# Kernel optimization log

Hardware: AMD Instinct MI355X
Metric: run time of the kernel (lower is better)

The kernel has to match this reference:

```python
import jax, jax.numpy as jnp
import numpy as np
from jax import lax

B, N, T, E, HE, HD, NE = 512, 100, 100, 128, 64, 256, 512
BETA = 0.25


def setup_inputs() -> dict:
    key = jax.random.key(0)
    ks = jax.random.split(key, 16)
    f32 = jnp.float32
    x = jax.random.normal(ks[0], (B, N, T), f32)
    traj_mask = (jax.random.uniform(ks[1], (B, N, T)) > 0.1).astype(f32)
    instance_mask = (jax.random.uniform(ks[2], (B, N)) > 0.2).astype(f32)

    def w_init(k, shape, fan_in):
        return (jax.random.normal(k, shape, f32) / np.sqrt(fan_in)).astype(f32)

    params = dict(
        conv1_w=w_init(ks[3], (HE, 2, 3), 2 * 3), conv1_b=jnp.zeros((HE,), f32),
        conv2_w=w_init(ks[4], (HE, HE, 3), HE * 3), conv2_b=jnp.zeros((HE,), f32),
        lat_w=w_init(ks[5], (E, HE), HE), lat_b=jnp.zeros((E,), f32),
        codebook=(jax.random.uniform(ks[6], (NE, E), f32) * 2.0 - 1.0) / NE,
        d1_w=w_init(ks[7], (HD, E), E), d1_b=jnp.zeros((HD,), f32),
        d2_w=w_init(ks[8], (HD, HD), HD), d2_b=jnp.zeros((HD,), f32),
        d3_w=w_init(ks[9], (T, HD), HD), d3_b=jnp.zeros((T,), f32),
    )
    return {"x": x, "traj_mask": traj_mask, "instance_mask": instance_mask, **params}


def _conv1d(h, w, b):
    # h: (M, C_in, L), w: (C_out, C_in, K) -> (M, C_out, L), padding=1 == SAME for K=3
    y = lax.conv_general_dilated(h, w, (1,), 'SAME', dimension_numbers=('NCH', 'OIH', 'NCH'))
    return jax.nn.relu(y + b[None, :, None])


def reference(x, traj_mask, instance_mask, conv1_w, conv1_b, conv2_w, conv2_b,
              lat_w, lat_b, codebook, d1_w, d1_b, d2_w, d2_b, d3_w, d3_b):
    b, n, t = x.shape
    steps = t // 2
    im = instance_mask[..., None]  # (B,N,1)

    # ---- encode (masked input) ----
    x_in = x * traj_mask * im
    h = x_in.reshape(b * n, steps, 2).transpose(0, 2, 1)  # (M, 2, steps)
    h = _conv1d(h, conv1_w, conv1_b)
    h = _conv1d(h, conv2_w, conv2_b)
    h = h.mean(axis=-1)                                   # (M, HE)
    z = (h @ lat_w.T + lat_b).reshape(b, n, -1)           # (B, N, E)
    z = z * im

    # ---- vector quantize (nbooks=1), quant_prop=1.0 ----
    zf = z.reshape(-1, z.shape[-1])                       # (M, E)
    d = ((zf * zf).sum(-1, keepdims=True)
         - 2.0 * zf @ codebook.T
         + (codebook * codebook).sum(-1))                 # (M, NE)
    idx = jnp.argmin(d, axis=-1)                          # (M,)
    zq = codebook[idx]                                    # (M, E) gather
    sg = lax.stop_gradient
    vq_loss = (BETA * jnp.mean((zf - sg(zq)) ** 2, -1)
               + jnp.mean((sg(zf) - zq) ** 2, -1)).reshape(b, n)
    zq = zf + sg(zq - zf)                                 # straight-through
    z_q = zq.reshape(b, n, -1)

    # ---- apply instance mask to VQ outputs ----
    denom = jnp.maximum(instance_mask.sum(), 1.0)
    vq_reduced = (vq_loss * instance_mask).sum() / denom
    indices = idx.reshape(b, n, 1)
    indices = jnp.where(im > 0, indices, jnp.full_like(indices, -1))
    z_q = z_q * im

    # ---- decode ----
    h2 = jax.nn.relu(z_q.reshape(b * n, -1) @ d1_w.T + d1_b)
    h2 = jax.nn.relu(h2 @ d2_w.T + d2_b)
    x_hat = (h2 @ d3_w.T + d3_b).reshape(b, n, t)

    # ---- masked reconstruction loss ----
    recon_w = im * traj_mask
    recon_loss = (((x_hat - x) ** 2) * recon_w).sum() / jnp.maximum(recon_w.sum(), 1.0)
    return x_hat, recon_loss, vq_reduced, indices
```

## Files before the change

### kernel.cpp

```cpp
#include <hip/hip_runtime.h>
#include <stdint.h>

typedef unsigned long long u64;
typedef unsigned short ushort_t;
typedef __attribute__((ext_vector_type(8))) short short8;
typedef __attribute__((ext_vector_type(8))) _Float16 half8;
typedef __attribute__((ext_vector_type(16))) float f32x16;


#define WS_RNP0     0ll
#define WS_RNP1     51200ll
#define WS_ZHI      102400ll
#define WS_ZLO      3379200ll
#define WS_ENCBHI   6656000ll
#define WS_ENCBLO   6662144ll
#define WS_CBHI     6668288ll
#define WS_CBLO     6701056ll
#define WS_CBNORM   6733824ll
#define WS_D1F      6734336ll
#define WS_D2F      6750720ll
#define WS_D3F      6783488ll
#define WS_ACCUMS   6799872ll
#define WS_GBEST    6799880ll
#define WS_H1       6902280ll
#define WS_H2       13455880ll

__device__ __host__ inline ushort_t bf16_rn(float v) {
  unsigned u = __float_as_uint(v);
  unsigned r = (u + 0x7fffu + ((u >> 16) & 1u)) >> 16;
  return (ushort_t)r;
}
union h2u { _Float16 h; unsigned short u; };
union s2h { short8 s; half8 h; };

__device__ inline unsigned pk2_bf16(float a, float b) {
  unsigned r;
  asm("v_cvt_pk_bf16_f32 %0, %1, %2" : "=v"(r) : "v"(a), "v"(b));
  return r;
}

__device__ inline int rowfn(int r, int half) { return (r & 3) + 8*(r >> 2) + 4*half; }

#define MFMA_BF16 __builtin_amdgcn_mfma_f32_32x32x16_bf16

__global__ __launch_bounds__(256) void prep_kernel(
    const float* __restrict__ w2, const float* __restrict__ cb,
    const float* __restrict__ d1w, const float* __restrict__ d2w,
    const float* __restrict__ d3w,
    ushort_t* __restrict__ ebhi, ushort_t* __restrict__ eblo,
    ushort_t* __restrict__ cbhi, ushort_t* __restrict__ cblo,
    ushort_t* __restrict__ d1f, ushort_t* __restrict__ d2f,
    ushort_t* __restrict__ d3f, float* __restrict__ cbnorm)
{
  const int total = 12288 + 65536 + 32768 + 65536 + 32768 + 512;
  for (int i = blockIdx.x*256 + threadIdx.x; i < total; i += gridDim.x*256) {
    int idx = i;
    if (idx < 12288) {
      int j = idx & 7, l6 = (idx >> 3) & 63, f = idx >> 9;
      int kt = f & 3, ntt = (f >> 2) & 1, t = f >> 3;
      int oc = ntt*32 + (l6 & 31);
      int ic = kt*16 + (l6 >> 5)*8 + j;
      float v = w2[(oc*64 + ic)*3 + t];
      ushort_t hi = bf16_rn(v);
      float hf = __uint_as_float(((unsigned)hi) << 16);
      ebhi[idx] = hi; eblo[idx] = bf16_rn(v - hf); continue;
    }
    idx -= 12288;
    if (idx < 65536) {
      int j = idx & 7, l6 = (idx >> 3) & 63, f = idx >> 9;
      int kt = f & 7, ntg = f >> 3;
      int k = kt*16 + (l6 >> 5)*8 + j;
      int n = ntg*32 + (l6 & 31);
      float v = cb[n*128 + k] * 512.0f;
      h2u a, b; a.h = (_Float16)v;
      b.h = (_Float16)(v - (float)a.h);
      cbhi[idx] = a.u; cblo[idx] = b.u; continue;
    }
    idx -= 65536;
    if (idx < 32768) {
      int j = idx & 7, l6 = (idx >> 3) & 63, f = idx >> 9;
      int kt = f & 7, ntg = f >> 3;
      int k = kt*16 + (l6 >> 5)*8 + j;
      int n = ntg*32 + (l6 & 31);
      d1f[idx] = bf16_rn(d1w[n*128 + k]); continue;
    }
    idx -= 32768;
    if (idx < 65536) {
      int j = idx & 7, l6 = (idx >> 3) & 63, f = idx >> 9;
      int kt = f & 15, ntg = f >> 4;
      int k = kt*16 + (l6 >> 5)*8 + j;
      int n = ntg*32 + (l6 & 31);
      d2f[idx] = bf16_rn(d2w[n*256 + k]); continue;
    }
    idx -= 65536;
    if (idx < 32768) {
      int j = idx & 7, l6 = (idx >> 3) & 63, f = idx >> 9;
      int kt = f & 15, ntg = f >> 4;
      int k = kt*16 + (l6 >> 5)*8 + j;
      int n = ntg*32 + (l6 & 31);
      d3f[idx] = (n < 100) ? bf16_rn(d3w[n*256 + k]) : (ushort_t)0; continue;
    }
    idx -= 32768;
    { double s = 0.0; const float* c = cb + idx*128;
      for (int e = 0; e < 128; ++e) { double v = (double)c[e]; s += v*v; }
      cbnorm[idx] = (float)s; }
  }
}

__global__ __launch_bounds__(256, 3) void encoder_kernel(
    const float* __restrict__ x, const float* __restrict__ tm,
    const float* __restrict__ imask,
    const float* w1, const float* b1,
    const ushort_t* __restrict__ ebhi, const ushort_t* __restrict__ eblo,
    const float* b2, float* __restrict__ red)
{
  __shared__ ushort_t s_H[4][52*128];
  const int tid  = threadIdx.x;
  const int wv   = __builtin_amdgcn_readfirstlane((int)(tid >> 6));
  const int lane = tid & 63;
  const int ln31 = lane & 31, half = lane >> 5;
  const long m   = (long)blockIdx.x*4 + wv;
  const float imv = imask[m];
  ushort_t* Hw  = s_H[wv];

  {
    const int p = (lane < 50) ? lane : 0;
    const long xb = m*100 + 2*p;
    const float2 x0v = *(const float2*)(x + xb);
    const float2 t0v = *(const float2*)(tm + xb);
    float2 xmv = {0.f, 0.f}, tmv = {0.f, 0.f};
    float2 xpv = {0.f, 0.f}, tpv = {0.f, 0.f};
    if (p > 0)  { xmv = *(const float2*)(x + xb - 2); tmv = *(const float2*)(tm + xb - 2); }
    if (p < 49) { xpv = *(const float2*)(x + xb + 2); tpv = *(const float2*)(tm + xb + 2); }
    const float a0 = xmv.x*tmv.x, c0 = xmv.y*tmv.y;
    const float a1 = x0v.x*t0v.x, c1 = x0v.y*t0v.y;
    const float a2 = xpv.x*tpv.x, c2 = xpv.y*tpv.y;
    const int row = lane + 1;
    const int sw  = (row & 7) << 4;
    char* rbase = (char*)(Hw + row*128);
    #pragma unroll
    for (int g = 0; g < 4; ++g) {
      unsigned hi8[8], lo8[8];
      #pragma unroll
      for (int pr = 0; pr < 8; ++pr) {
        const int o = g*16 + pr*2;
        const float* wA = w1 + (long)o*6;
        const float* wB = wA + 6;
        float sA = 0.f, sB = 0.f;
        sA = fmaf(wA[0], a0, sA); sA = fmaf(wA[1], a1, sA); sA = fmaf(wA[2], a2, sA);
        sA = fmaf(wA[3], c0, sA); sA = fmaf(wA[4], c1, sA); sA = fmaf(wA[5], c2, sA);
        sB = fmaf(wB[0], a0, sB); sB = fmaf(wB[1], a1, sB); sB = fmaf(wB[2], a2, sB);
        sB = fmaf(wB[3], c0, sB); sB = fmaf(wB[4], c1, sB); sB = fmaf(wB[5], c2, sB);
        const float hA = fmaxf(fmaf(imv, sA, b1[o]),     0.f);
        const float hB = fmaxf(fmaf(imv, sB, b1[o + 1]), 0.f);
        const unsigned h = pk2_bf16(hA, hB);
        const float ha = __uint_as_float(h << 16);
        const float hb = __uint_as_float(h & 0xffff0000u);
        lo8[pr] = pk2_bf16(hA - ha, hB - hb);
        hi8[pr] = h;
      }
      if (lane < 50) {
        *(short8*)(rbase + ((g*32)       ^ sw)) = *(short8*)&hi8[0];
        *(short8*)(rbase + ((g*32 + 16)  ^ sw)) = *(short8*)&hi8[4];
        *(short8*)(rbase + (128 + ((g*32)      ^ sw))) = *(short8*)&lo8[0];
        *(short8*)(rbase + (128 + ((g*32 + 16) ^ sw))) = *(short8*)&lo8[4];
      }
    }
    if (lane == 50 || lane == 51) {
      const int zr = (lane == 50) ? 0 : 51;
      short8 z8 = {};
      short8* d = (short8*)(Hw + zr*128);
      #pragma unroll
      for (int i = 0; i < 16; ++i) d[i] = z8;
    }
  }
  asm volatile("s_waitcnt lgkmcnt(0)" ::: "memory");
  __builtin_amdgcn_sched_barrier(0);

  f32x16 acc00, acc01, acc10, acc11;
  #pragma unroll
  for (int q = 0; q < 16; ++q) { acc00[q] = 0.f; acc01[q] = 0.f; acc10[q] = 0.f; acc11[q] = 0.f; }
  {
    const short8* bh8 = (const short8*)ebhi;
    const short8* bl8 = (const short8*)eblo;
    for (int t = 0; t < 3; ++t) {
      const int r0 = ln31 + t;
      int r1 = 32 + ln31 + t;
      if (r1 > 51) r1 = 51;
      const int sw0 = (r0 & 7) << 4, sw1 = (r1 & 7) << 4;
      const char* b0p = (const char*)(Hw + r0*128);
      const char* b1p = (const char*)(Hw + r1*128);
      #pragma unroll
      for (int kt = 0; kt < 4; ++kt) {
        const int f0 = (t*2 + 0)*4 + kt;
        const int f1 = (t*2 + 1)*4 + kt;
        const int offh = kt*32 + half*16;
        const short8 Bh0 = bh8[f0*64 + lane], Bl0 = bl8[f0*64 + lane];
        const short8 Bh1 = bh8[f1*64 + lane], Bl1 = bl8[f1*64 + lane];
        const short8 ah0 = *(const short8*)(b0p + (offh ^ sw0));
        const short8 al0 = *(const short8*)(b0p + (128 + (offh ^ sw0)));
        const short8 ah1 = *(const short8*)(b1p + (offh ^ sw1));
        const short8 al1 = *(const short8*)(b1p + (128 + (offh ^ sw1)));
        acc00 = MFMA_BF16(ah0, Bh0, acc00, 0, 0, 0);
        acc00 = MFMA_BF16(ah0, Bl0, acc00, 0, 0, 0);
        acc00 = MFMA_BF16(al0, Bh0, acc00, 0, 0, 0);
        acc01 = MFMA_BF16(ah0, Bh1, acc01, 0, 0, 0);
        acc01 = MFMA_BF16(ah0, Bl1, acc01, 0, 0, 0);
        acc01 = MFMA_BF16(al0, Bh1, acc01, 0, 0, 0);
        acc10 = MFMA_BF16(ah1, Bh0, acc10, 0, 0, 0);
        acc10 = MFMA_BF16(ah1, Bl0, acc10, 0, 0, 0);
        acc10 = MFMA_BF16(al1, Bh0, acc10, 0, 0, 0);
        acc11 = MFMA_BF16(ah1, Bh1, acc11, 0, 0, 0);
        acc11 = MFMA_BF16(ah1, Bl1, acc11, 0, 0, 0);
        acc11 = MFMA_BF16(al1, Bh1, acc11, 0, 0, 0);
      }
    }
  }

  {
    const float bv0 = b2[ln31];
    const float bv1 = b2[32 + ln31];
    float s0 = 0.f, s1 = 0.f;
    #pragma unroll
    for (int r = 0; r < 16; ++r) {
      s0 += fmaxf(acc00[r] + bv0, 0.f);
      s1 += fmaxf(acc01[r] + bv1, 0.f);
      const int mpos = 32 + rowfn(r, half);
      const float v10 = fmaxf(acc10[r] + bv0, 0.f);
      const float v11 = fmaxf(acc11[r] + bv1, 0.f);
      if (mpos < 50) { s0 += v10; s1 += v11; }
    }
    s0 += __shfl_xor(s0, 32);
    s1 += __shfl_xor(s1, 32);
    if (half == 0) {
      red[m*64 + ln31]      = s0;
      red[m*64 + 32 + ln31] = s1;
    }
  }
}

__global__ __launch_bounds__(256, 4) void latent_kernel(
    const float* __restrict__ red, const float* __restrict__ imask,
    const float* __restrict__ latw, const float* __restrict__ latb,
    ushort_t* __restrict__ zhi, ushort_t* __restrict__ zlo,
    float* __restrict__ rnp0, float* __restrict__ rnp1)
{
  __shared__ float s_r[64*64];
  __shared__ float s_im[64];
  const int tid = threadIdx.x;
  const long m0 = (long)blockIdx.x * 64;
  {
    const int r = tid >> 2, seg = tid & 3;
    const float4* src = (const float4*)(red + (m0 + r)*64 + seg*16);
    float4* dst = (float4*)(s_r + r*64 + seg*16);
    dst[0] = src[0]; dst[1] = src[1]; dst[2] = src[2]; dst[3] = src[3];
  }
  if (tid < 64) s_im[tid] = imask[m0 + tid];
  __syncthreads();

  const int e = tid & 127, mh = tid >> 7;
  const int lane = tid & 63;
  float4 W[16];
  const float4* wp = (const float4*)(latw + (long)e*64);
  #pragma unroll
  for (int q = 0; q < 16; ++q) W[q] = wp[q];
  const float lb = latb[e];

  for (int i = 0; i < 32; ++i) {
    const int ml = mh*32 + i;
    const float4* rp = (const float4*)(s_r + ml*64);
    float a = 0.f;
    #pragma unroll
    for (int q = 0; q < 16; ++q) {
      const float4 r4 = rp[q];
      a = fmaf(W[q].x, r4.x, a); a = fmaf(W[q].y, r4.y, a);
      a = fmaf(W[q].z, r4.z, a); a = fmaf(W[q].w, r4.w, a);
    }
    const float z = fmaf(0.02f, a, lb) * s_im[ml];
    h2u zh, zl; zh.h = (_Float16)z; zl.h = (_Float16)(z - (float)zh.h);
    const long mg = m0 + ml;
    zhi[mg*128 + e] = zh.u;
    zlo[mg*128 + e] = zl.u;
    float v = z*z;
    #pragma unroll
    for (int off = 32; off > 0; off >>= 1) v += __shfl_down(v, off);
    if (lane == 0) { if (e < 64) rnp0[mg] = v; else rnp1[mg] = v; }
  }
}

__global__ __launch_bounds__(256) void vq_kernel(
    const ushort_t* __restrict__ zhi, const ushort_t* __restrict__ zlo,
    const ushort_t* __restrict__ cbhi, const ushort_t* __restrict__ cblo,
    const float* __restrict__ rnp0, const float* __restrict__ rnp1,
    const float* __restrict__ cbnorm, u64* __restrict__ gbest)
{
  __shared__ ushort_t s_ah[32*136];
  __shared__ ushort_t s_al[32*136];
  __shared__ float s_rn[32];
  __shared__ u64 s_best[32];
  const int tid = threadIdx.x;
  const int m0 = blockIdx.x * 32;
  {
    const short8* gh = (const short8*)(zhi + (long)m0*128);
    const short8* gl = (const short8*)(zlo + (long)m0*128);
    const int row = tid >> 3, c8 = (tid & 7)*2;
    ((short8*)s_ah)[row*17 + c8]     = gh[tid*2];
    ((short8*)s_ah)[row*17 + c8 + 1] = gh[tid*2 + 1];
    ((short8*)s_al)[row*17 + c8]     = gl[tid*2];
    ((short8*)s_al)[row*17 + c8 + 1] = gl[tid*2 + 1];
  }
  if (tid < 32) { s_rn[tid] = rnp0[m0 + tid] + rnp1[m0 + tid]; s_best[tid] = ~0ULL; }
  __syncthreads();

  const int wv = tid >> 6, lane = tid & 63;
  const int ln31 = lane & 31, half = lane >> 5;
  float rnv[16];
  #pragma unroll
  for (int r = 0; r < 16; ++r) rnv[r] = s_rn[rowfn(r, half)];

  u64 best[16];
  #pragma unroll
  for (int r = 0; r < 16; ++r) best[r] = ~0ULL;

  const short8* ch8 = (const short8*)cbhi;
  const short8* cl8 = (const short8*)cblo;
  for (int ct = 0; ct < 4; ++ct) {
    const int ntg = wv*4 + ct;
    half8 Bh[8], Bl[8];
    #pragma unroll
    for (int kt = 0; kt < 8; ++kt) {
      s2h a, b;
      a.s = ch8[(ntg*8 + kt)*64 + lane];
      b.s = cl8[(ntg*8 + kt)*64 + lane];
      Bh[kt] = a.h; Bl[kt] = b.h;
    }
    f32x16 acc;
    #pragma unroll
    for (int q = 0; q < 16; ++q) acc[q] = 0.f;
    const int base8 = ln31*17 + half;
    #pragma unroll
    for (int kt = 0; kt < 8; ++kt) {
      s2h ah, al;
      ah.s = ((const short8*)s_ah)[base8 + kt*2];
      al.s = ((const short8*)s_al)[base8 + kt*2];
      acc = __builtin_amdgcn_mfma_f32_32x32x16_f16(ah.h, Bh[kt], acc, 0, 0, 0);
      acc = __builtin_amdgcn_mfma_f32_32x32x16_f16(ah.h, Bl[kt], acc, 0, 0, 0);
      acc = __builtin_amdgcn_mfma_f32_32x32x16_f16(al.h, Bh[kt], acc, 0, 0, 0);
    }
    const int code = ntg*32 + ln31;
    const float nrm = cbnorm[code];
    #pragma unroll
    for (int r = 0; r < 16; ++r) {
      const float t = fmaf(-0.00390625f, acc[r], rnv[r]);
      const float d = t + nrm;
      const u64 pk = ((u64)__float_as_uint(d) << 32) | (u64)(unsigned)code;
      if (pk < best[r]) best[r] = pk;
    }
  }
  #pragma unroll
  for (int r = 0; r < 16; ++r) atomicMin(&s_best[rowfn(r, half)], best[r]);
  __syncthreads();
  if (tid < 32) gbest[m0 + tid] = s_best[tid];
}

__global__ __launch_bounds__(256) void dec1_kernel(
    const float* __restrict__ cb, const u64* __restrict__ gbest,
    const float* __restrict__ imask, const ushort_t* __restrict__ bfrag,
    const float* __restrict__ bias, ushort_t* __restrict__ h1out,
    float* __restrict__ out_idx, float* __restrict__ accums)
{
  __shared__ ushort_t s_a[64*136];
  __shared__ int s_idx[64];
  __shared__ float s_act[64];
  const int tid = threadIdx.x;
  const long m0 = (long)blockIdx.x * 64;
  if (tid < 64) {
    const u64 pk = gbest[m0 + tid];
    const int ii = (int)(unsigned)(pk & 0xffffffffULL);
    const float dd = __uint_as_float((unsigned)(pk >> 32));
    const float imv = imask[m0 + tid];
    s_idx[tid] = ii; s_act[tid] = imv;
    out_idx[m0 + tid] = (imv > 0.f) ? (float)ii : -1.0f;
    float vqp = 1.25f * dd * (1.0f/128.0f) * imv;
    float sim = imv;
    #pragma unroll
    for (int off = 32; off > 0; off >>= 1) {
      vqp += __shfl_down(vqp, off); sim += __shfl_down(sim, off);
    }
    if (tid == 0) { atomicAdd(&accums[1], vqp); atomicAdd(&accums[3], sim); }
  }
  __syncthreads();
  {
    const int row = tid >> 2, seg = tid & 3;
    const float4* src = (const float4*)(cb + (long)s_idx[row]*128 + seg*32);
    const float im = s_act[row];
    ushort_t tmp[32];
    #pragma unroll
    for (int q = 0; q < 8; ++q) {
      const float4 v = src[q];
      tmp[q*4+0] = bf16_rn(v.x*im); tmp[q*4+1] = bf16_rn(v.y*im);
      tmp[q*4+2] = bf16_rn(v.z*im); tmp[q*4+3] = bf16_rn(v.w*im);
    }
    short8* dst = (short8*)(s_a + row*136 + seg*32);
    #pragma unroll
    for (int q = 0; q < 4; ++q) dst[q] = *(short8*)&tmp[q*8];
  }
  __syncthreads();
  const int wv = tid >> 6, lane = tid & 63;
  const int ln31 = lane & 31, half = lane >> 5;
  const short8* bf = (const short8*)bfrag;
  #pragma unroll
  for (int nti = 0; nti < 2; ++nti) {
    const int ntg = wv + nti*4;
    short8 B[8];
    #pragma unroll
    for (int kt = 0; kt < 8; ++kt) B[kt] = bf[(ntg*8 + kt)*64 + lane];
    const float bv = bias[ntg*32 + ln31];
    #pragma unroll
    for (int mtl = 0; mtl < 2; ++mtl) {
      f32x16 acc;
      #pragma unroll
      for (int q = 0; q < 16; ++q) acc[q] = 0.f;
      const int base8 = (mtl*32 + ln31)*17 + half;
      #pragma unroll
      for (int kt = 0; kt < 8; ++kt) {
        const short8 a = ((const short8*)s_a)[base8 + kt*2];
        acc = MFMA_BF16(a, B[kt], acc, 0, 0, 0);
      }
      const int col = ntg*32 + ln31;
      #pragma unroll
      for (int r = 0; r < 16; ++r) {
        const long row = m0 + mtl*32 + rowfn(r, half);
        h1out[row*256 + col] = bf16_rn(fmaxf(acc[r] + bv, 0.f));
      }
    }
  }
}

__global__ __launch_bounds__(256) void dec2_kernel(
    const ushort_t* __restrict__ ain, const ushort_t* __restrict__ bfrag,
    const float* __restrict__ bias, ushort_t* __restrict__ outbuf)
{
  __shared__ ushort_t s_a[64*264];
  const int tid = threadIdx.x;
  const long m0 = (long)blockIdx.x * 64;
  {
    const int row = tid >> 2, seg = tid & 3;
    const short8* src = (const short8*)(ain + (m0 + row)*256 + seg*64);
    short8* dst = (short8*)(s_a + row*264 + seg*64);
    #pragma unroll
    for (int q = 0; q < 8; ++q) dst[q] = src[q];
  }
  __syncthreads();
  const int wv = tid >> 6, lane = tid & 63;
  const int ln31 = lane & 31, half = lane >> 5;
  const short8* bf = (const short8*)bfrag;
  #pragma unroll
  for (int nti = 0; nti < 2; ++nti) {
    const int ntg = wv + nti*4;
    short8 B[16];
    #pragma unroll
    for (int kt = 0; kt < 16; ++kt) B[kt] = bf[(ntg*16 + kt)*64 + lane];
    const float bv = bias[ntg*32 + ln31];
    #pragma unroll
    for (int mtl = 0; mtl < 2; ++mtl) {
      f32x16 acc;
      #pragma unroll
      for (int q = 0; q < 16; ++q) acc[q] = 0.f;
      const int base8 = (mtl*32 + ln31)*33 + half;
      #pragma unroll
      for (int kt = 0; kt < 16; ++kt) {
        const short8 a = ((const short8*)s_a)[base8 + kt*2];
        acc = MFMA_BF16(a, B[kt], acc, 0, 0, 0);
      }
      const int col = ntg*32 + ln31;
      #pragma unroll
      for (int r = 0; r < 16; ++r) {
        const long row = m0 + mtl*32 + rowfn(r, half);
        outbuf[row*256 + col] = bf16_rn(fmaxf(acc[r] + bv, 0.f));
      }
    }
  }
}

__global__ __launch_bounds__(256) void dec3_kernel(
    const ushort_t* __restrict__ ain, const ushort_t* __restrict__ bfrag,
    const float* __restrict__ bias, const float* __restrict__ x,
    const float* __restrict__ tm, const float* __restrict__ imask,
    float* __restrict__ xhat, float* __restrict__ accums)
{
  __shared__ ushort_t s_a[64*264];
  const int tid = threadIdx.x;
  const long m0 = (long)blockIdx.x * 64;
  {
    const int row = tid >> 2, seg = tid & 3;
    const short8* src = (const short8*)(ain + (m0 + row)*256 + seg*64);
    short8* dst = (short8*)(s_a + row*264 + seg*64);
    #pragma unroll
    for (int q = 0; q < 8; ++q) dst[q] = src[q];
  }
  __syncthreads();
  const int wv = tid >> 6, lane = tid & 63;
  const int ln31 = lane & 31, half = lane >> 5;
  const short8* bf = (const short8*)bfrag;
  const int ntg = wv;
  short8 B[16];
  #pragma unroll
  for (int kt = 0; kt < 16; ++kt) B[kt] = bf[(ntg*16 + kt)*64 + lane];
  const int col = ntg*32 + ln31;
  const float bv = (col < 100) ? bias[col] : 0.f;
  float part = 0.f, wsum = 0.f;
  #pragma unroll
  for (int mtl = 0; mtl < 2; ++mtl) {
    f32x16 acc;
    #pragma unroll
    for (int q = 0; q < 16; ++q) acc[q] = 0.f;
    const int base8 = (mtl*32 + ln31)*33 + half;
    #pragma unroll
    for (int kt = 0; kt < 16; ++kt) {
      const short8 a = ((const short8*)s_a)[base8 + kt*2];
      acc = MFMA_BF16(a, B[kt], acc, 0, 0, 0);
    }
    if (col < 100) {
      #pragma unroll
      for (int r = 0; r < 16; ++r) {
        const long row = m0 + mtl*32 + rowfn(r, half);
        const float xh = acc[r] + bv;
        xhat[row*100 + col] = xh;
        const float wgt = imask[row] * tm[row*100 + col];
        const float df = xh - x[row*100 + col];
        part = fmaf(df*df, wgt, part);
        wsum += wgt;
      }
    }
  }
  #pragma unroll
  for (int off = 32; off > 0; off >>= 1) {
    part += __shfl_down(part, off); wsum += __shfl_down(wsum, off);
  }
  __shared__ float s_p[4], s_w[4];
  if (lane == 0) { s_p[wv] = part; s_w[wv] = wsum; }
  __syncthreads();
  if (tid == 0) {
    atomicAdd(&accums[0], s_p[0]+s_p[1]+s_p[2]+s_p[3]);
    atomicAdd(&accums[2], s_w[0]+s_w[1]+s_w[2]+s_w[3]);
  }
}

__global__ void finalize_kernel(const float* __restrict__ accums, float* __restrict__ out) {
  if (threadIdx.x == 0 && blockIdx.x == 0) {
    out[5120000] = accums[0] / fmaxf(accums[2], 1.0f);
    out[5120001] = accums[1] / fmaxf(accums[3], 1.0f);
  }
}

extern "C" void kernel_launch(void* const* d_in, const int* in_sizes, int n_in,
                              void* d_out, int out_size, void* d_ws, size_t ws_size,
                              hipStream_t stream)
{
  (void)in_sizes; (void)n_in; (void)out_size; (void)ws_size;
  const float* x     = (const float*)d_in[0];
  const float* tmsk  = (const float*)d_in[1];
  const float* imask = (const float*)d_in[2];
  const float* w1    = (const float*)d_in[3];
  const float* b1    = (const float*)d_in[4];
  const float* w2    = (const float*)d_in[5];
  const float* b2    = (const float*)d_in[6];
  const float* latw  = (const float*)d_in[7];
  const float* latb  = (const float*)d_in[8];
  const float* cb    = (const float*)d_in[9];
  const float* d1w   = (const float*)d_in[10];
  const float* d1b   = (const float*)d_in[11];
  const float* d2w   = (const float*)d_in[12];
  const float* d2b   = (const float*)d_in[13];
  const float* d3w   = (const float*)d_in[14];
  const float* d3b   = (const float*)d_in[15];
  float* out = (float*)d_out;
  float* ws  = (float*)d_ws;

  float*    rnp0   = ws + WS_RNP0;
  float*    rnp1   = ws + WS_RNP1;
  ushort_t* zhi    = (ushort_t*)(ws + WS_ZHI);
  ushort_t* zlo    = (ushort_t*)(ws + WS_ZLO);
  ushort_t* ebhi   = (ushort_t*)(ws + WS_ENCBHI);
  ushort_t* eblo   = (ushort_t*)(ws + WS_ENCBLO);
  ushort_t* cbhi   = (ushort_t*)(ws + WS_CBHI);
  ushort_t* cblo   = (ushort_t*)(ws + WS_CBLO);
  float*    cbnorm = ws + WS_CBNORM;
  ushort_t* d1f    = (ushort_t*)(ws + WS_D1F);
  ushort_t* d2f    = (ushort_t*)(ws + WS_D2F);
  ushort_t* d3f    = (ushort_t*)(ws + WS_D3F);
  float*    accums = ws + WS_ACCUMS;
  u64*      gbest  = (u64*)(ws + WS_GBEST);
  ushort_t* h1     = (ushort_t*)(ws + WS_H1);
  ushort_t* h2     = (ushort_t*)(ws + WS_H2);
  float*    red    = ws + WS_H1;
  float* xhat    = out;
  float* out_idx = out + 5120002;

  hipMemsetAsync(accums, 0, 8*sizeof(float), stream);

  prep_kernel<<<512, 256, 0, stream>>>(w2, cb, d1w, d2w, d3w,
                                       ebhi, eblo, cbhi, cblo, d1f, d2f, d3f, cbnorm);
  encoder_kernel<<<12800, 256, 0, stream>>>(x, tmsk, imask, w1, b1, ebhi, eblo, b2, red);
  latent_kernel<<<800, 256, 0, stream>>>(red, imask, latw, latb, zhi, zlo, rnp0, rnp1);
  vq_kernel<<<1600, 256, 0, stream>>>(zhi, zlo, cbhi, cblo, rnp0, rnp1, cbnorm, gbest);
  dec1_kernel<<<800, 256, 0, stream>>>(cb, gbest, imask, d1f, d1b, h1, out_idx, accums);
  dec2_kernel<<<800, 256, 0, stream>>>(h1, d2f, d2b, h2);
  dec3_kernel<<<800, 256, 0, stream>>>(h2, d3f, d3b, x, tmsk, imask, xhat, accums);
  finalize_kernel<<<1, 64, 0, stream>>>(accums, out);
}
```

Measured before the change: 479.8 us.

## Fuse three decoder GEMM kernels into one LDS-resident decoder kernel

Merges dec1, dec2 and dec3 into a single kernel that keeps the 64-row h1 and h2 activations in shared memory instead of writing and rereading them through global memory, which also removes two kernel launches. It also changes the encoder's LDS swizzle to XOR bit 7 by row, so the lo-half stores and loads sit in a different bank pattern and may conflict less. The fused kernel uses about 67KB of LDS per block and declares a minimum of two blocks per CU, which may limit occupancy compared with the separate kernels.

```diff
diff --git a/kernel.cpp b/kernel.cpp
--- a/kernel.cpp
+++ b/kernel.cpp
@@ -22,8 +22,7 @@
 #define WS_D3F      6783488ll
 #define WS_ACCUMS   6799872ll
 #define WS_GBEST    6799880ll
-#define WS_H1       6902280ll
-#define WS_H2       13455880ll
+#define WS_RED      6902280ll
 
 __device__ __host__ inline ushort_t bf16_rn(float v) {
   unsigned u = __float_as_uint(v);
@@ -136,7 +135,7 @@
     const float a1 = x0v.x*t0v.x, c1 = x0v.y*t0v.y;
     const float a2 = xpv.x*tpv.x, c2 = xpv.y*tpv.y;
     const int row = lane + 1;
-    const int sw  = (row & 7) << 4;
+    const int sw  = ((row & 7) << 4) | (((row >> 3) & 1) << 7);
     char* rbase = (char*)(Hw + row*128);
     #pragma unroll
     for (int g = 0; g < 4; ++g) {
@@ -160,10 +159,10 @@
         hi8[pr] = h;
       }
       if (lane < 50) {
-        *(short8*)(rbase + ((g*32)       ^ sw)) = *(short8*)&hi8[0];
-        *(short8*)(rbase + ((g*32 + 16)  ^ sw)) = *(short8*)&hi8[4];
-        *(short8*)(rbase + (128 + ((g*32)      ^ sw))) = *(short8*)&lo8[0];
-        *(short8*)(rbase + (128 + ((g*32 + 16) ^ sw))) = *(short8*)&lo8[4];
+        *(short8*)(rbase + ((g*32)        ^ sw)) = *(short8*)&hi8[0];
+        *(short8*)(rbase + ((g*32 + 16)   ^ sw)) = *(short8*)&hi8[4];
+        *(short8*)(rbase + ((g*32 + 128)  ^ sw)) = *(short8*)&lo8[0];
+        *(short8*)(rbase + ((g*32 + 144)  ^ sw)) = *(short8*)&lo8[4];
       }
     }
     if (lane == 50 || lane == 51) {
@@ -187,7 +186,8 @@
       const int r0 = ln31 + t;
       int r1 = 32 + ln31 + t;
       if (r1 > 51) r1 = 51;
-      const int sw0 = (r0 & 7) << 4, sw1 = (r1 & 7) << 4;
+      const int sw0 = ((r0 & 7) << 4) | (((r0 >> 3) & 1) << 7);
+      const int sw1 = ((r1 & 7) << 4) | (((r1 >> 3) & 1) << 7);
       const char* b0p = (const char*)(Hw + r0*128);
       const char* b1p = (const char*)(Hw + r1*128);
       #pragma unroll
@@ -198,9 +198,9 @@
         const short8 Bh0 = bh8[f0*64 + lane], Bl0 = bl8[f0*64 + lane];
         const short8 Bh1 = bh8[f1*64 + lane], Bl1 = bl8[f1*64 + lane];
         const short8 ah0 = *(const short8*)(b0p + (offh ^ sw0));
-        const short8 al0 = *(const short8*)(b0p + (128 + (offh ^ sw0)));
+        const short8 al0 = *(const short8*)(b0p + ((offh + 128) ^ sw0));
         const short8 ah1 = *(const short8*)(b1p + (offh ^ sw1));
-        const short8 al1 = *(const short8*)(b1p + (128 + (offh ^ sw1)));
+        const short8 al1 = *(const short8*)(b1p + ((offh + 128) ^ sw1));
         acc00 = MFMA_BF16(ah0, Bh0, acc00, 0, 0, 0);
         acc00 = MFMA_BF16(ah0, Bl0, acc00, 0, 0, 0);
         acc00 = MFMA_BF16(al0, Bh0, acc00, 0, 0, 0);
@@ -363,17 +363,24 @@
   if (tid < 32) gbest[m0 + tid] = s_best[tid];
 }
 
-__global__ __launch_bounds__(256) void dec1_kernel(
+__global__ __launch_bounds__(256, 2) void decoder_kernel(
     const float* __restrict__ cb, const u64* __restrict__ gbest,
-    const float* __restrict__ imask, const ushort_t* __restrict__ bfrag,
-    const float* __restrict__ bias, ushort_t* __restrict__ h1out,
-    float* __restrict__ out_idx, float* __restrict__ accums)
+    const float* __restrict__ imask,
+    const ushort_t* __restrict__ d1frag, const float* __restrict__ d1b,
+    const ushort_t* __restrict__ d2frag, const float* __restrict__ d2b,
+    const ushort_t* __restrict__ d3frag, const float* __restrict__ d3b,
+    const float* __restrict__ x, const float* __restrict__ tm,
+    float* __restrict__ xhat, float* __restrict__ out_idx,
+    float* __restrict__ accums)
 {
-  __shared__ ushort_t s_a[64*136];
+  __shared__ ushort_t s_u[64*264];
+  __shared__ ushort_t s_h1[64*264];
   __shared__ int s_idx[64];
   __shared__ float s_act[64];
+  __shared__ float s_p[4], s_w[4];
   const int tid = threadIdx.x;
   const long m0 = (long)blockIdx.x * 64;
+
   if (tid < 64) {
     const u64 pk = gbest[m0 + tid];
     const int ii = (int)(unsigned)(pk & 0xffffffffULL);
@@ -401,149 +408,120 @@
       tmp[q*4+0] = bf16_rn(v.x*im); tmp[q*4+1] = bf16_rn(v.y*im);
       tmp[q*4+2] = bf16_rn(v.z*im); tmp[q*4+3] = bf16_rn(v.w*im);
     }
-    short8* dst = (short8*)(s_a + row*136 + seg*32);
+    short8* dst = (short8*)(s_u + row*136 + seg*32);
     #pragma unroll
     for (int q = 0; q < 4; ++q) dst[q] = *(short8*)&tmp[q*8];
   }
   __syncthreads();
+
   const int wv = tid >> 6, lane = tid & 63;
   const int ln31 = lane & 31, half = lane >> 5;
-  const short8* bf = (const short8*)bfrag;
-  #pragma unroll
-  for (int nti = 0; nti < 2; ++nti) {
-    const int ntg = wv + nti*4;
-    short8 B[8];
-    #pragma unroll
-    for (int kt = 0; kt < 8; ++kt) B[kt] = bf[(ntg*8 + kt)*64 + lane];
-    const float bv = bias[ntg*32 + ln31];
+
+  {
+    const short8* bf = (const short8*)d1frag;
+    #pragma unroll
+    for (int nti = 0; nti < 2; ++nti) {
+      const int ntg = wv + nti*4;
+      short8 B[8];
+      #pragma unroll
+      for (int kt = 0; kt < 8; ++kt) B[kt] = bf[(ntg*8 + kt)*64 + lane];
+      const float bv = d1b[ntg*32 + ln31];
+      #pragma unroll
+      for (int mtl = 0; mtl < 2; ++mtl) {
+        f32x16 acc;
+        #pragma unroll
+        for (int q = 0; q < 16; ++q) acc[q] = 0.f;
+        const int base8 = (mtl*32 + ln31)*17 + half;
+        #pragma unroll
+        for (int kt = 0; kt < 8; ++kt) {
+          const short8 a = ((const short8*)s_u)[base8 + kt*2];
+          acc = MFMA_BF16(a, B[kt], acc, 0, 0, 0);
+        }
+        const int col = ntg*32 + ln31;
+        #pragma unroll
+        for (int r = 0; r < 16; ++r) {
+          const int row = mtl*32 + rowfn(r, half);
+          s_h1[row*264 + col] = bf16_rn(fmaxf(acc[r] + bv, 0.f));
+        }
+      }
+    }
+  }
+  __syncthreads();
+
+  {
+    const short8* bf = (const short8*)d2frag;
+    #pragma unroll
+    for (int nti = 0; nti < 2; ++nti) {
+      const int ntg = wv + nti*4;
+      short8 B[16];
+      #pragma unroll
+      for (int kt = 0; kt < 16; ++kt) B[kt] = bf[(ntg*16 + kt)*64 + lane];
+      const float bv = d2b[ntg*32 + ln31];
+      #pragma unroll
+      for (int mtl = 0; mtl < 2; ++mtl) {
+        f32x16 acc;
+        #pragma unroll
+        for (int q = 0; q < 16; ++q) acc[q] = 0.f;
+        const int base8 = (mtl*32 + ln31)*33 + half;
+        #pragma unroll
+        for (int kt = 0; kt < 16; ++kt) {
+          const short8 a = ((const short8*)s_h1)[base8 + kt*2];
+          acc = MFMA_BF16(a, B[kt], acc, 0, 0, 0);
+        }
+        const int col = ntg*32 + ln31;
+        #pragma unroll
+        for (int r = 0; r < 16; ++r) {
+          const int row = mtl*32 + rowfn(r, half);
+          s_u[row*264 + col] = bf16_rn(fmaxf(acc[r] + bv, 0.f));
+        }
+      }
+    }
+  }
+  __syncthreads();
+
+  {
+    const short8* bf = (const short8*)d3frag;
+    const int ntg = wv;
+    short8 B[16];
+    #pragma unroll
+    for (int kt = 0; kt < 16; ++kt) B[kt] = bf[(ntg*16 + kt)*64 + lane];
+    const int col = ntg*32 + ln31;
+    const float bv = (col < 100) ? d3b[col] : 0.f;
+    float part = 0.f, wsum = 0.f;
     #pragma unroll
     for (int mtl = 0; mtl < 2; ++mtl) {
       f32x16 acc;
       #pragma unroll
       for (int q = 0; q < 16; ++q) acc[q] = 0.f;
-      const int base8 = (mtl*32 + ln31)*17 + half;
-      #pragma unroll
-      for (int kt = 0; kt < 8; ++kt) {
-        const short8 a = ((const short8*)s_a)[base8 + kt*2];
+      const int base8 = (mtl*32 + ln31)*33 + half;
+      #pragma unroll
+      for (int kt = 0; kt < 16; ++kt) {
+        const short8 a = ((const short8*)s_u)[base8 + kt*2];
         acc = MFMA_BF16(a, B[kt], acc, 0, 0, 0);
       }
-      const int col = ntg*32 + ln31;
-      #pragma unroll
-      for (int r = 0; r < 16; ++r) {
-        const long row = m0 + mtl*32 + rowfn(r, half);
-        h1out[row*256 + col] = bf16_rn(fmaxf(acc[r] + bv, 0.f));
-      }
-    }
-  }
-}
-
-__global__ __launch_bounds__(256) void dec2_kernel(
-    const ushort_t* __restrict__ ain, const ushort_t* __restrict__ bfrag,
-    const float* __restrict__ bias, ushort_t* __restrict__ outbuf)
-{
-  __shared__ ushort_t s_a[64*264];
-  const int tid = threadIdx.x;
-  const long m0 = (long)blockIdx.x * 64;
-  {
-    const int row = tid >> 2, seg = tid & 3;
-    const short8* src = (const short8*)(ain + (m0 + row)*256 + seg*64);
-    short8* dst = (short8*)(s_a + row*264 + seg*64);
-    #pragma unroll
-    for (int q = 0; q < 8; ++q) dst[q] = src[q];
-  }
-  __syncthreads();
-  const int wv = tid >> 6, lane = tid & 63;
-  const int ln31 = lane & 31, half = lane >> 5;
-  const short8* bf = (const short8*)bfrag;
-  #pragma unroll
-  for (int nti = 0; nti < 2; ++nti) {
-    const int ntg = wv + nti*4;
-    short8 B[16];
-    #pragma unroll
-    for (int kt = 0; kt < 16; ++kt) B[kt] = bf[(ntg*16 + kt)*64 + lane];
-    const float bv = bias[ntg*32 + ln31];
-    #pragma unroll
-    for (int mtl = 0; mtl < 2; ++mtl) {
-      f32x16 acc;
-      #pragma unroll
-      for (int q = 0; q < 16; ++q) acc[q] = 0.f;
-      const int base8 = (mtl*32 + ln31)*33 + half;
-      #pragma unroll
-      for (int kt = 0; kt < 16; ++kt) {
-        const short8 a = ((const short8*)s_a)[base8 + kt*2];
-        acc = MFMA_BF16(a, B[kt], acc, 0, 0, 0);
-      }
-      const int col = ntg*32 + ln31;
-      #pragma unroll
-      for (int r = 0; r < 16; ++r) {
-        const long row = m0 + mtl*32 + rowfn(r, half);
-        outbuf[row*256 + col] = bf16_rn(fmaxf(acc[r] + bv, 0.f));
-      }
-    }
-  }
-}
-
-__global__ __launch_bounds__(256) void dec3_kernel(
-    const ushort_t* __restrict__ ain, const ushort_t* __restrict__ bfrag,
-    const float* __restrict__ bias, const float* __restrict__ x,
-    const float* __restrict__ tm, const float* __restrict__ imask,
-    float* __restrict__ xhat, float* __restrict__ accums)
-{
-  __shared__ ushort_t s_a[64*264];
-  const int tid = threadIdx.x;
-  const long m0 = (long)blockIdx.x * 64;
-  {
-    const int row = tid >> 2, seg = tid & 3;
-    const short8* src = (const short8*)(ain + (m0 + row)*256 + seg*64);
-    short8* dst = (short8*)(s_a + row*264 + seg*64);
-    #pragma unroll
-    for (int q = 0; q < 8; ++q) dst[q] = src[q];
-  }
-  __syncthreads();
-  const int wv = tid >> 6, lane = tid & 63;
-  const int ln31 = lane & 31, half = lane >> 5;
-  const short8* bf = (const short8*)bfrag;
-  const int ntg = wv;
-  short8 B[16];
-  #pragma unroll
-  for (int kt = 0; kt < 16; ++kt) B[kt] = bf[(ntg*16 + kt)*64 + lane];
-  const int col = ntg*32 + ln31;
-  const float bv = (col < 100) ? bias[col] : 0.f;
-  float part = 0.f, wsum = 0.f;
-  #pragma unroll
-  for (int mtl = 0; mtl < 2; ++mtl) {
-    f32x16 acc;
-    #pragma unroll
-    for (int q = 0; q < 16; ++q) acc[q] = 0.f;
-    const int base8 = (mtl*32 + ln31)*33 + half;
-    #pragma unroll
-    for (int kt = 0; kt < 16; ++kt) {
-      const short8 a = ((const short8*)s_a)[base8 + kt*2];
-      acc = MFMA_BF16(a, B[kt], acc, 0, 0, 0);
-    }
-    if (col < 100) {
-      #pragma unroll
-      for (int r = 0; r < 16; ++r) {
-        const long row = m0 + mtl*32 + rowfn(r, half);
-        const float xh = acc[r] + bv;
-        xhat[row*100 + col] = xh;
-        const float wgt = imask[row] * tm[row*100 + col];
-        const float df = xh - x[row*100 + col];
-        part = fmaf(df*df, wgt, part);
-        wsum += wgt;
-      }
-    }
-  }
-  #pragma unroll
-  for (int off = 32; off > 0; off >>= 1) {
-    part += __shfl_down(part, off); wsum += __shfl_down(wsum, off);
-  }
-  __shared__ float s_p[4], s_w[4];
-  if (lane == 0) { s_p[wv] = part; s_w[wv] = wsum; }
-  __syncthreads();
-  if (tid == 0) {
-    atomicAdd(&accums[0], s_p[0]+s_p[1]+s_p[2]+s_p[3]);
-    atomicAdd(&accums[2], s_w[0]+s_w[1]+s_w[2]+s_w[3]);
+      if (col < 100) {
+        #pragma unroll
+        for (int r = 0; r < 16; ++r) {
+          const long row = m0 + mtl*32 + rowfn(r, half);
+          const float xh = acc[r] + bv;
+          xhat[row*100 + col] = xh;
+          const float wgt = imask[row] * tm[row*100 + col];
+          const float df = xh - x[row*100 + col];
+          part = fmaf(df*df, wgt, part);
+          wsum += wgt;
+        }
+      }
+    }
+    #pragma unroll
+    for (int off = 32; off > 0; off >>= 1) {
+      part += __shfl_down(part, off); wsum += __shfl_down(wsum, off);
+    }
+    if (lane == 0) { s_p[wv] = part; s_w[wv] = wsum; }
+    __syncthreads();
+    if (tid == 0) {
+      atomicAdd(&accums[0], s_p[0]+s_p[1]+s_p[2]+s_p[3]);
+      atomicAdd(&accums[2], s_w[0]+s_w[1]+s_w[2]+s_w[3]);
+    }
   }
 }
 
@@ -592,9 +570,7 @@
   ushort_t* d3f    = (ushort_t*)(ws + WS_D3F);
   float*    accums = ws + WS_ACCUMS;
   u64*      gbest  = (u64*)(ws + WS_GBEST);
-  ushort_t* h1     = (ushort_t*)(ws + WS_H1);
-  ushort_t* h2     = (ushort_t*)(ws + WS_H2);
-  float*    red    = ws + WS_H1;
+  float*    red    = ws + WS_RED;
   float* xhat    = out;
   float* out_idx = out + 5120002;
 
@@ -605,8 +581,7 @@
   encoder_kernel<<<12800, 256, 0, stream>>>(x, tmsk, imask, w1, b1, ebhi, eblo, b2, red);
   latent_kernel<<<800, 256, 0, stream>>>(red, imask, latw, latb, zhi, zlo, rnp0, rnp1);
   vq_kernel<<<1600, 256, 0, stream>>>(zhi, zlo, cbhi, cblo, rnp0, rnp1, cbnorm, gbest);
-  dec1_kernel<<<800, 256, 0, stream>>>(cb, gbest, imask, d1f, d1b, h1, out_idx, accums);
-  dec2_kernel<<<800, 256, 0, stream>>>(h1, d2f, d2b, h2);
-  dec3_kernel<<<800, 256, 0, stream>>>(h2, d3f, d3b, x, tmsk, imask, xhat, accums);
+  decoder_kernel<<<800, 256, 0, stream>>>(cb, gbest, imask, d1f, d1b, d2f, d2b,
+                                          d3f, d3b, x, tmsk, xhat, out_idx, accums);
   finalize_kernel<<<1, 64, 0, stream>>>(accums, out);
 }
```

New measurement: 437.0 us. -8.9%, faster.
